# Performance work log

Hardware: AMD Instinct MI355X
Metric: run time of the kernel (lower is better)

The kernel has to match this reference:

```python
import jax, jax.numpy as jnp
import numpy as np

BUCKET_BINS = np.array([0, 1, 2, 3, 4, 5, 7, 8, 15, 16, 31, 32, 63, 64], dtype=np.int32)
MAX_WINDOW = 8  # args.span_maximum_length


def _span_index_table(L):
    # Static enumeration of all spans of width 1..MAX_WINDOW (stride-1 unfold).
    starts, ends = [], []
    for w in range(1, min(L, MAX_WINDOW) + 1):
        s = np.arange(0, L - w + 1)
        starts.append(s)
        ends.append(s + w)
    return (np.concatenate(starts).astype(np.int32),
            np.concatenate(ends).astype(np.int32))


def _bucket(width):
    # index of last bin with width >= bin value
    return jnp.searchsorted(jnp.asarray(BUCKET_BINS), width, side='right') - 1


def _fnn(h, W1, b1, W2, b2, W3, b3):
    # Linear->ReLU->(Dropout: eval identity)->Linear->ReLU->Linear->Softmax
    h = jax.nn.relu(h @ W1 + b1)
    h = jax.nn.relu(h @ W2 + b2)
    return jax.nn.softmax(h @ W3 + b3, axis=-1)


def setup_inputs() -> dict:
    key = jax.random.key(0)
    ks = jax.random.split(key, 16)
    B, L, D = 8, 256, 768
    H, WD, DD = 1024, 25, 25
    span_dim = 2 * D + WD          # 1561
    pair_dim = 2 * span_dim + DD   # 3147
    f = jnp.float32

    def g(k, shape, scale):
        return jax.random.normal(k, shape, dtype=f) * scale

    return {
        'x': g(ks[0], (B, L, D), 1.0),
        'width_emb': g(ks[1], (len(BUCKET_BINS), WD), 0.02),
        'dist_emb': g(ks[2], (len(BUCKET_BINS), DD), 0.02),
        'Ws1': g(ks[3], (span_dim, H), 0.02), 'bs1': jnp.zeros((H,), f),
        'Ws2': g(ks[4], (H, H), 0.02), 'bs2': jnp.zeros((H,), f),
        'Ws3': g(ks[5], (H, 3), 0.02), 'bs3': jnp.zeros((3,), f),
        'Wp1': g(ks[6], (pair_dim, H), 0.02), 'bp1': jnp.zeros((H,), f),
        'Wp2': g(ks[7], (H, H), 0.02), 'bp2': jnp.zeros((H,), f),
        'Wp3': g(ks[8], (H, 4), 0.02), 'bp3': jnp.zeros((4,), f),
        'nz': 64,
    }


def reference(x, width_emb, dist_emb, Ws1, bs1, Ws2, bs2, Ws3, bs3,
              Wp1, bp1, Wp2, bp2, Wp3, bp3, nz):
    B, L, D = x.shape
    starts_np, ends_np = _span_index_table(L)
    starts = jnp.asarray(starts_np)
    ends = jnp.asarray(ends_np)

    # ---- SpanRepresentation: [start token, end token, width bucket emb] ----
    w_emb = width_emb[_bucket(ends - starts)]                     # [S, WD]
    spans = jnp.concatenate([
        x[:, starts_np, :],                                       # [B,S,D]
        x[:, ends_np - 1, :],                                     # [B,S,D]
        jnp.broadcast_to(w_emb, (B,) + w_emb.shape),              # [B,S,WD]
    ], axis=-1)                                                   # [B,S,span_dim]

    # ---- span_fnn + PrunedTargetOpinion (top-k on aspect/opinion probs) ----
    span_prob = _fnn(spans, Ws1, bs1, Ws2, bs2, Ws3, bs3)         # [B,S,3]
    _, t_idx = jax.lax.top_k(span_prob[:, :, 1], nz)              # aspect  [B,nz]
    _, o_idx = jax.lax.top_k(span_prob[:, :, 2], nz)              # opinion [B,nz]

    # ---- PairRepresentation: all target x opinion pairs ----
    t_rep = jnp.take_along_axis(spans, t_idx[:, :, None], axis=1) # [B,nz,sd]
    o_rep = jnp.take_along_axis(spans, o_idx[:, :, None], axis=1)
    ta, tb = starts[t_idx], ends[t_idx]                           # [B,nz]
    oc, od = starts[o_idx], ends[o_idx]
    # min_distance(a,b,c,d) = min(|b-c|, |a-d|)
    dist = jnp.minimum(jnp.abs(tb[:, :, None] - oc[:, None, :]),
                       jnp.abs(ta[:, :, None] - od[:, None, :]))  # [B,nz,nz]
    d_emb = dist_emb[_bucket(dist)]                               # [B,nz,nz,DD]
    sd = spans.shape[-1]
    pairs = jnp.concatenate([
        jnp.broadcast_to(t_rep[:, :, None, :], (B, nz, nz, sd)),
        jnp.broadcast_to(o_rep[:, None, :, :], (B, nz, nz, sd)),
        d_emb,
    ], axis=-1).reshape(B, nz * nz, 2 * sd + d_emb.shape[-1])     # [B,nz^2,pair_dim]

    pair_prob = _fnn(pairs, Wp1, bp1, Wp2, bp2, Wp3, bp3)         # [B,nz^2,4]
    return span_prob, pair_prob
```

## Files before the change

kernel.cpp:

```cpp
#include <hip/hip_runtime.h>
#include <cstdint>
#include <cstddef>

#define BATCH 8
#define SEQ   256
#define DIM   768
#define NSPAN 2020
#define HID   1024
#define NZ    64

typedef unsigned short u16;
typedef unsigned int   u32;
typedef unsigned long long u64;

typedef __bf16 bf16x8 __attribute__((ext_vector_type(8)));
typedef float  f32x4  __attribute__((ext_vector_type(4)));

__device__ __forceinline__ u16 f2bf(float f) {
    union { float f; u32 u; } x; x.f = f;
    u32 r = x.u + 0x7fffu + ((x.u >> 16) & 1u);
    return (u16)(r >> 16);
}
__device__ __forceinline__ float bf2f(u16 b) {
    union { u32 u; float f; } x; x.u = ((u32)b) << 16;
    return x.f;
}
__device__ __forceinline__ void splitbf(float v, u16& h, u16& l) {
    h = f2bf(v);
    l = f2bf(v - bf2f(h));
}

__device__ __forceinline__ void gld_lds16(const void* g, void* l) {
    __builtin_amdgcn_global_load_lds(
        (const __attribute__((address_space(1))) unsigned int*)g,
        (__attribute__((address_space(3))) unsigned int*)l, 16, 0, 0);
}

__device__ __forceinline__ void span_decode(int s, int& start, int& end, int& w) {
    int off = 0;
#pragma unroll
    for (int wi = 1; wi <= 8; ++wi) {
        int cnt = SEQ - wi + 1;
        if (s < off + cnt) { w = wi; start = s - off; end = start + wi; return; }
        off += cnt;
    }
    w = 8; start = 0; end = 8;
}

__device__ __forceinline__ int dbucket(int d) {
    int b = 0;
    b += (d >= 1);  b += (d >= 2);  b += (d >= 3);  b += (d >= 4);
    b += (d >= 5);  b += (d >= 7);  b += (d >= 8);  b += (d >= 15);
    b += (d >= 16); b += (d >= 31); b += (d >= 32); b += (d >= 63);
    b += (d >= 64);
    return b;
}

__device__ __forceinline__ void xcd_map(int L, int sft, int& bx, int& by) {
    int grp = L >> (3 + sft);
    int rem = L & ((1 << (3 + sft)) - 1);
    bx = rem >> 3;
    by = (grp << 3) | (rem & 7);
}

__global__ __launch_bounds__(256) void k_prep(
    const float* __restrict__ x,  u16* __restrict__ xh,   u16* __restrict__ xl,
    const float* __restrict__ wemb, const float* __restrict__ demb,
    const float* __restrict__ bs1, const float* __restrict__ bp1,
    float* __restrict__ wtabS, float* __restrict__ wtabPt,
    float* __restrict__ wtabPo, float* __restrict__ dtab,
    const float* __restrict__ Ws1, u16* __restrict__ W1Th, u16* __restrict__ W1Tl,
    const float* __restrict__ Ws2, u16* __restrict__ W2Th, u16* __restrict__ W2Tl,
    const float* __restrict__ Wp2, u16* __restrict__ Wp2T,
    const float* __restrict__ Wp1, u16* __restrict__ Wp1T4)
{
    __shared__ float tile[32][33];
    const int bid = blockIdx.x, tid = threadIdx.x;
    if (bid < 6144) {
        int i = bid * 256 + tid;
        u16 h, l; splitbf(x[i], h, l);
        xh[i] = h; xl[i] = l;
        return;
    }
    if (bid < 6296) {
        int t = bid - 6144;
        int row = t >> 2;
        int h = (t & 3) * 256 + tid;
        const int wb[8] = {1,2,3,4,5,5,6,7};
        if (row < 8) {
            int bk = wb[row];
            float acc = bs1[h];
            for (int j = 0; j < 25; ++j) acc = fmaf(wemb[bk*25+j], Ws1[(size_t)(1536+j)*HID + h], acc);
            wtabS[row*HID + h] = acc;
        } else if (row < 16) {
            int bk = wb[row-8];
            float acc = 0.f;
            for (int j = 0; j < 25; ++j) acc = fmaf(wemb[bk*25+j], Wp1[(size_t)(1536+j)*HID + h], acc);
            wtabPt[(row-8)*HID + h] = acc;
        } else if (row < 24) {
            int bk = wb[row-16];
            float acc = 0.f;
            for (int j = 0; j < 25; ++j) acc = fmaf(wemb[bk*25+j], Wp1[(size_t)(3097+j)*HID + h], acc);
            wtabPo[(row-16)*HID + h] = acc;
        } else {
            int tt = row - 24;
            float acc = bp1[h];
            for (int j = 0; j < 25; ++j) acc = fmaf(demb[tt*25+j], Wp1[(size_t)(3122+j)*HID + h], acc);
            dtab[tt*HID + h] = acc;
        }
        return;
    }
    const int tb = bid - 6296;
    const int tr = tid >> 3;
    const int tc4 = (tid & 7) * 4;
    int job, tk, tn, blk = 0;
    if (tb < 1536)      { job = 0; tk = tb % 24; tn = tb / 24; }
    else if (tb < 2560) { job = 1; int t = tb - 1536; tk = t & 31; tn = t >> 5; }
    else if (tb < 3584) { job = 2; int t = tb - 2560; tk = t & 31; tn = t >> 5; }
    else                { job = 3; int t = tb - 3584; blk = t / 768; int r = t - blk * 768; tk = r % 24; tn = r / 24; }
    const int k0 = tk * 32, n0 = tn * 32;

    int k = k0 + tr;
    float4 v;
    if (job == 0) {
        const float* s = (n0 < 1024) ? (Ws1 + (size_t)k * HID + n0)
                                     : (Ws1 + (size_t)(768 + k) * HID + (n0 - 1024));
        v = *(const float4*)(s + tc4);
    } else if (job == 1) {
        v = *(const float4*)(Ws2 + (size_t)k * HID + n0 + tc4);
    } else if (job == 2) {
        v = *(const float4*)(Wp2 + (size_t)k * HID + n0 + tc4);
    } else {
        const int roff[4] = {0, 768, 1561, 2329};
        v = *(const float4*)(Wp1 + (size_t)(roff[blk] + k) * HID + n0 + tc4);
    }
    tile[tr][tc4+0] = v.x; tile[tr][tc4+1] = v.y;
    tile[tr][tc4+2] = v.z; tile[tr][tc4+3] = v.w;
    __syncthreads();

    int nn = n0 + tr;
    float w0 = tile[tc4+0][tr], w1 = tile[tc4+1][tr];
    float w2 = tile[tc4+2][tr], w3 = tile[tc4+3][tr];
    if (job == 0) {
        size_t d = (size_t)nn * 768 + k0 + tc4;
        u16 h0,l0,h1,l1,h2,l2,h3,l3;
        splitbf(w0,h0,l0); splitbf(w1,h1,l1); splitbf(w2,h2,l2); splitbf(w3,h3,l3);
        *(uint2*)(W1Th + d) = make_uint2((u32)h0 | ((u32)h1 << 16), (u32)h2 | ((u32)h3 << 16));
        *(uint2*)(W1Tl + d) = make_uint2((u32)l0 | ((u32)l1 << 16), (u32)l2 | ((u32)l3 << 16));
    } else if (job == 1) {
        size_t d = (size_t)nn * 1024 + k0 + tc4;
        u16 h0,l0,h1,l1,h2,l2,h3,l3;
        splitbf(w0,h0,l0); splitbf(w1,h1,l1); splitbf(w2,h2,l2); splitbf(w3,h3,l3);
        *(uint2*)(W2Th + d) = make_uint2((u32)h0 | ((u32)h1 << 16), (u32)h2 | ((u32)h3 << 16));
        *(uint2*)(W2Tl + d) = make_uint2((u32)l0 | ((u32)l1 << 16), (u32)l2 | ((u32)l3 << 16));
    } else if (job == 2) {
        size_t d = (size_t)nn * 1024 + k0 + tc4;
        *(uint2*)(Wp2T + d) = make_uint2((u32)f2bf(w0) | ((u32)f2bf(w1) << 16),
                                         (u32)f2bf(w2) | ((u32)f2bf(w3) << 16));
    } else {
        size_t d = (size_t)blk * 786432 + (size_t)nn * 768 + k0 + tc4;
        *(uint2*)(Wp1T4 + d) = make_uint2((u32)f2bf(w0) | ((u32)f2bf(w1) << 16),
                                          (u32)f2bf(w2) | ((u32)f2bf(w3) << 16));
    }
}

__global__ __launch_bounds__(256) void k_gemm3bf(
    const u16* __restrict__ Ah, const u16* __restrict__ Al, int lda,
    const u16* __restrict__ BTh, const u16* __restrict__ BTl, int ldb,
    float* __restrict__ C, int ldc,
    int M, int K, int nby, int sft)
{
    int bx, by;
    xcd_map(blockIdx.x, sft, bx, by);
    if (by >= nby) return;
    __shared__ __align__(16) u16 sm[4 * 128 * 32];
    u16* sAh = sm;
    u16* sAl = sm + 4096;
    u16* sBh = sm + 8192;
    u16* sBl = sm + 12288;
    const int tid = threadIdx.x;
    const int bm = by * 128, bn = bx * 128;
    const int wave = tid >> 6, lane = tid & 63;
    const int wr = wave >> 1, wc = wave & 1;
    const int q = lane >> 4, tl = lane & 15;

    f32x4 zero = {0.f, 0.f, 0.f, 0.f};
    f32x4 acc[4][4];
#pragma unroll
    for (int i = 0; i < 4; ++i)
#pragma unroll
        for (int j = 0; j < 4; ++j) acc[i][j] = zero;

    const int srow = lane >> 2;
    const int scol = (lane & 3) * 8;
    int ra0 = bm + wave * 32 + srow;      if (ra0 >= M) ra0 = M - 1;
    int ra1 = bm + wave * 32 + 16 + srow; if (ra1 >= M) ra1 = M - 1;
    const int rb0 = bn + wave * 32 + srow;
    const int rb1 = bn + wave * 32 + 16 + srow;
    u16* dA0 = sAh + wave * 1024;  u16* dA1 = dA0 + 512;
    u16* dL0 = sAl + wave * 1024;  u16* dL1 = dL0 + 512;
    u16* dB0 = sBh + wave * 1024;  u16* dB1 = dB0 + 512;
    u16* dC0 = sBl + wave * 1024;  u16* dC1 = dC0 + 512;
    const u16* gA0 = Ah  + (size_t)ra0 * lda + scol;
    const u16* gA1 = Ah  + (size_t)ra1 * lda + scol;
    const u16* gL0 = Al  + (size_t)ra0 * lda + scol;
    const u16* gL1 = Al  + (size_t)ra1 * lda + scol;
    const u16* gB0 = BTh + (size_t)rb0 * ldb + scol;
    const u16* gB1 = BTh + (size_t)rb1 * ldb + scol;
    const u16* gC0 = BTl + (size_t)rb0 * ldb + scol;
    const u16* gC1 = BTl + (size_t)rb1 * ldb + scol;

    for (int k0 = 0; k0 < K; k0 += 32) {
        gld_lds16(gA0 + k0, dA0);
        gld_lds16(gA1 + k0, dA1);
        gld_lds16(gL0 + k0, dL0);
        gld_lds16(gL1 + k0, dL1);
        gld_lds16(gB0 + k0, dB0);
        gld_lds16(gB1 + k0, dB1);
        gld_lds16(gC0 + k0, dC0);
        gld_lds16(gC1 + k0, dC1);
        __syncthreads();
        bf16x8 ah[4], al[4], bh[4], bl[4];
#pragma unroll
        for (int t = 0; t < 4; ++t) {
            int arow = (wr*64 + t*16 + tl) * 32 + q*8;
            int brow = (wc*64 + t*16 + tl) * 32 + q*8;
            ah[t] = *(const bf16x8*)(&sAh[arow]);
            al[t] = *(const bf16x8*)(&sAl[arow]);
            bh[t] = *(const bf16x8*)(&sBh[brow]);
            bl[t] = *(const bf16x8*)(&sBl[brow]);
        }
#pragma unroll
        for (int ti = 0; ti < 4; ++ti)
#pragma unroll
            for (int tj = 0; tj < 4; ++tj) {
                acc[ti][tj] = __builtin_amdgcn_mfma_f32_16x16x32_bf16(ah[ti], bh[tj], acc[ti][tj], 0, 0, 0);
                acc[ti][tj] = __builtin_amdgcn_mfma_f32_16x16x32_bf16(al[ti], bh[tj], acc[ti][tj], 0, 0, 0);
                acc[ti][tj] = __builtin_amdgcn_mfma_f32_16x16x32_bf16(ah[ti], bl[tj], acc[ti][tj], 0, 0, 0);
            }
        __syncthreads();
    }
#pragma unroll
    for (int ti = 0; ti < 4; ++ti) {
#pragma unroll
        for (int tj = 0; tj < 4; ++tj) {
            int gcol = bn + wc*64 + tj*16 + tl;
#pragma unroll
            for (int r = 0; r < 4; ++r) {
                int grow = bm + wr*64 + ti*16 + q*4 + r;
                if (grow >= M) continue;
                C[(size_t)grow * ldc + gcol] = acc[ti][tj][r];
            }
        }
    }
}

__global__ __launch_bounds__(256) void k_span_l2(
    const u16* __restrict__ Ah, const u16* __restrict__ Al,
    const u16* __restrict__ BTh, const u16* __restrict__ BTl,
    const float* __restrict__ bs2, const float* __restrict__ Ws3,
    float* __restrict__ part, int M)
{
    int bx, by;
    xcd_map(blockIdx.x, 3, bx, by);
    if (by >= 127) return;
    __shared__ __align__(16) u16 sm[4 * 128 * 32];
    u16* sAh = sm;
    u16* sAl = sm + 4096;
    u16* sBh = sm + 8192;
    u16* sBl = sm + 12288;
    const int tid = threadIdx.x;
    const int bm = by * 128, bn = bx * 128;
    const int wave = tid >> 6, lane = tid & 63;
    const int wr = wave >> 1, wc = wave & 1;
    const int q = lane >> 4, tl = lane & 15;

    f32x4 zero = {0.f, 0.f, 0.f, 0.f};
    f32x4 acc[4][4];
#pragma unroll
    for (int i = 0; i < 4; ++i)
#pragma unroll
        for (int j = 0; j < 4; ++j) acc[i][j] = zero;

    const int srow = lane >> 2;
    const int scol = (lane & 3) * 8;
    int ra0 = bm + wave * 32 + srow;      if (ra0 >= M) ra0 = M - 1;
    int ra1 = bm + wave * 32 + 16 + srow; if (ra1 >= M) ra1 = M - 1;
    const int rb0 = bn + wave * 32 + srow;
    const int rb1 = bn + wave * 32 + 16 + srow;
    u16* dA0 = sAh + wave * 1024;  u16* dA1 = dA0 + 512;
    u16* dL0 = sAl + wave * 1024;  u16* dL1 = dL0 + 512;
    u16* dB0 = sBh + wave * 1024;  u16* dB1 = dB0 + 512;
    u16* dC0 = sBl + wave * 1024;  u16* dC1 = dC0 + 512;
    const u16* gA0 = Ah  + (size_t)ra0 * HID + scol;
    const u16* gA1 = Ah  + (size_t)ra1 * HID + scol;
    const u16* gL0 = Al  + (size_t)ra0 * HID + scol;
    const u16* gL1 = Al  + (size_t)ra1 * HID + scol;
    const u16* gB0 = BTh + (size_t)rb0 * HID + scol;
    const u16* gB1 = BTh + (size_t)rb1 * HID + scol;
    const u16* gC0 = BTl + (size_t)rb0 * HID + scol;
    const u16* gC1 = BTl + (size_t)rb1 * HID + scol;

    for (int k0 = 0; k0 < HID; k0 += 32) {
        gld_lds16(gA0 + k0, dA0);
        gld_lds16(gA1 + k0, dA1);
        gld_lds16(gL0 + k0, dL0);
        gld_lds16(gL1 + k0, dL1);
        gld_lds16(gB0 + k0, dB0);
        gld_lds16(gB1 + k0, dB1);
        gld_lds16(gC0 + k0, dC0);
        gld_lds16(gC1 + k0, dC1);
        __syncthreads();
        bf16x8 ah[4], al[4], bh[4], bl[4];
#pragma unroll
        for (int t = 0; t < 4; ++t) {
            int arow = (wr*64 + t*16 + tl) * 32 + q*8;
            int brow = (wc*64 + t*16 + tl) * 32 + q*8;
            ah[t] = *(const bf16x8*)(&sAh[arow]);
            al[t] = *(const bf16x8*)(&sAl[arow]);
            bh[t] = *(const bf16x8*)(&sBh[brow]);
            bl[t] = *(const bf16x8*)(&sBl[brow]);
        }
#pragma unroll
        for (int ti = 0; ti < 4; ++ti)
#pragma unroll
            for (int tj = 0; tj < 4; ++tj) {
                acc[ti][tj] = __builtin_amdgcn_mfma_f32_16x16x32_bf16(ah[ti], bh[tj], acc[ti][tj], 0, 0, 0);
                acc[ti][tj] = __builtin_amdgcn_mfma_f32_16x16x32_bf16(al[ti], bh[tj], acc[ti][tj], 0, 0, 0);
                acc[ti][tj] = __builtin_amdgcn_mfma_f32_16x16x32_bf16(ah[ti], bl[tj], acc[ti][tj], 0, 0, 0);
            }
        __syncthreads();
    }
    const int slot = bx * 2 + wc;
#pragma unroll
    for (int ti = 0; ti < 4; ++ti) {
#pragma unroll
        for (int r = 0; r < 4; ++r) {
            int grow = bm + wr*64 + ti*16 + q*4 + r;
            float l0 = 0.f, l1 = 0.f, l2 = 0.f;
#pragma unroll
            for (int tj = 0; tj < 4; ++tj) {
                int gcol = bn + wc*64 + tj*16 + tl;
                float v = fmaxf(acc[ti][tj][r] + bs2[gcol], 0.f);
                const float* w3 = Ws3 + gcol * 3;
                l0 = fmaf(v, w3[0], l0);
                l1 = fmaf(v, w3[1], l1);
                l2 = fmaf(v, w3[2], l2);
            }
#pragma unroll
            for (int off = 8; off > 0; off >>= 1) {
                l0 += __shfl_down(l0, off, 16);
                l1 += __shfl_down(l1, off, 16);
                l2 += __shfl_down(l2, off, 16);
            }
            if (tl == 0 && grow < M) {
                float* dst = part + ((size_t)grow * 16 + slot) * 3;
                dst[0] = l0; dst[1] = l1; dst[2] = l2;
            }
        }
    }
}

__global__ __launch_bounds__(256) void k_pairL1(
    const u16* __restrict__ xh, const u16* __restrict__ Wp1T4,
    float* __restrict__ TO2, const int* __restrict__ toks)
{
    __shared__ __align__(16) u16 sm[2 * 64 * 32];
    u16* sA = sm;
    u16* sB = sm + 2048;
    const int tid = threadIdx.x;
    const int bid = blockIdx.x;
    const int p = bid >> 8;
    const int bx = bid & 15, by = (bid >> 4) & 15;
    const int bm = by * 64, bn = bx * 64;
    const int wave = tid >> 6, lane = tid & 63;
    const int wr = wave >> 1, wc = wave & 1;
    const int q = lane >> 4, tl = lane & 15;
    const bool isO = bm >= 512;

    f32x4 zero = {0.f, 0.f, 0.f, 0.f};
    f32x4 acc[2][2];
#pragma unroll
    for (int i = 0; i < 2; ++i)
#pragma unroll
        for (int j = 0; j < 2; ++j) acc[i][j] = zero;

    const int srow = tid >> 2;
    const int scol = (tid & 3) * 8;
    u16* dA = sA + wave * 512;
    u16* dB = sB + wave * 512;

    int arow = toks[bm + srow + p * 1024];
    const u16* gA = xh + (size_t)arow * DIM + scol;
    const u16* gB = Wp1T4 + ((size_t)((isO ? 2 : 0) + p) * 1024 + bn + srow) * DIM + scol;
    for (int k0 = 0; k0 < DIM; k0 += 32) {
        gld_lds16(gA + k0, dA);
        gld_lds16(gB + k0, dB);
        __syncthreads();
        bf16x8 af[2], bf[2];
#pragma unroll
        for (int t = 0; t < 2; ++t) {
            af[t] = *(const bf16x8*)(&sA[(wr*32 + t*16 + tl) * 32 + q*8]);
            bf[t] = *(const bf16x8*)(&sB[(wc*32 + t*16 + tl) * 32 + q*8]);
        }
#pragma unroll
        for (int ti = 0; ti < 2; ++ti)
#pragma unroll
            for (int tj = 0; tj < 2; ++tj)
                acc[ti][tj] = __builtin_amdgcn_mfma_f32_16x16x32_bf16(af[ti], bf[tj], acc[ti][tj], 0, 0, 0);
        __syncthreads();
    }
    float* dstb = TO2 + (size_t)p * 1024 * HID;
#pragma unroll
    for (int ti = 0; ti < 2; ++ti) {
#pragma unroll
        for (int tj = 0; tj < 2; ++tj) {
            int gcol = bn + wc*32 + tj*16 + tl;
#pragma unroll
            for (int r = 0; r < 4; ++r) {
                int grow = bm + wr*32 + ti*16 + q*4 + r;
                dstb[(size_t)grow * HID + gcol] = acc[ti][tj][r];
            }
        }
    }
}

__global__ __launch_bounds__(256) void k_build_h1s(
    const float* __restrict__ XALL, const float* __restrict__ wtabS,
    u16* __restrict__ h1h, u16* __restrict__ h1l)
{
    int r = blockIdx.x;
    int b = r / NSPAN, s = r - b * NSPAN;
    int st, en, w; span_decode(s, st, en, w);
    const float4* xs = (const float4*)(XALL + (size_t)(b*SEQ + st) * 2048);
    const float4* xe = (const float4*)(XALL + (size_t)(b*SEQ + en - 1) * 2048 + 1024);
    const float4* wt = (const float4*)(wtabS + (size_t)(w-1) * HID);
    int t = threadIdx.x;
    float4 a = xs[t], bz = xe[t], c = wt[t];
    float v0 = fmaxf(a.x + bz.x + c.x, 0.f);
    float v1 = fmaxf(a.y + bz.y + c.y, 0.f);
    float v2 = fmaxf(a.z + bz.z + c.z, 0.f);
    float v3 = fmaxf(a.w + bz.w + c.w, 0.f);
    u16 h0,l0,h1,l1,h2,l2,h3,l3;
    splitbf(v0,h0,l0); splitbf(v1,h1,l1); splitbf(v2,h2,l2); splitbf(v3,h3,l3);
    size_t base = (size_t)r * HID + t * 4;
    *(uint2*)(h1h + base) = make_uint2((u32)h0 | ((u32)h1 << 16), (u32)h2 | ((u32)h3 << 16));
    *(uint2*)(h1l + base) = make_uint2((u32)l0 | ((u32)l1 << 16), (u32)l2 | ((u32)l3 << 16));
}

__global__ __launch_bounds__(256) void k_topk(
    const float* __restrict__ partS, const float* __restrict__ bs3,
    float* __restrict__ out, int* __restrict__ t_idx, int* __restrict__ o_idx,
    int* __restrict__ toks)
{
    int b = blockIdx.x >> 1;
    int head = 1 + (blockIdx.x & 1);
    int* outp = (head == 1 ? t_idx : o_idx) + b * NZ;
    __shared__ u64 keys[2048];
    int tid = threadIdx.x;
#pragma unroll
    for (int ii = 0; ii < 8; ++ii) {
        int s = tid + ii * 256;
        u32 fb = 0;
        if (s < NSPAN) {
            const float* p = partS + (size_t)(b * NSPAN + s) * 48;
            float s0 = bs3[0], s1 = bs3[1], s2 = bs3[2];
#pragma unroll
            for (int t = 0; t < 16; ++t) {
                s0 += p[t*3]; s1 += p[t*3+1]; s2 += p[t*3+2];
            }
            float m = fmaxf(s0, fmaxf(s1, s2));
            float e0 = expf(s0 - m), e1 = expf(s1 - m), e2 = expf(s2 - m);
            float inv = 1.f / (e0 + e1 + e2);
            float p0 = e0 * inv, p1 = e1 * inv, p2 = e2 * inv;
            float* o = out + (size_t)(b * NSPAN + s) * 3;
            o[0] = p0; o[1] = p1; o[2] = p2;
            union { float f; u32 u; } x;
            x.f = (head == 1) ? p1 : p2;
            fb = x.u;
        }
        keys[s] = ((u64)fb << 32) | (u64)(0xFFFFFFFFu - (u32)s);
    }
    __syncthreads();
    for (int k = 2; k <= 2048; k <<= 1) {
        for (int j = k >> 1; j > 0; j >>= 1) {
#pragma unroll
            for (int ii = 0; ii < 8; ++ii) {
                int i = tid + ii * 256;
                int ixj = i ^ j;
                if (ixj > i) {
                    u64 a = keys[i], c = keys[ixj];
                    bool desc = (i & k) == 0;
                    bool wrong = desc ? (a < c) : (a > c);
                    if (wrong) { keys[i] = c; keys[ixj] = a; }
                }
            }
            __syncthreads();
        }
    }
    if (tid < NZ) {
        u64 key = keys[tid];
        int fi = (int)(0xFFFFFFFFu - (u32)(key & 0xFFFFFFFFu));
        if (fi < 0 || fi >= NSPAN) fi = 0;
        outp[tid] = fi;
        int st, en, w; span_decode(fi, st, en, w);
        int base = (head == 1 ? 0 : 512) + b * NZ + tid;
        toks[base] = b * SEQ + st;
        toks[1024 + base] = b * SEQ + en - 1;
    }
}

__global__ __launch_bounds__(256) void k_build_h1p(
    const float* __restrict__ TO2, const int* __restrict__ t_idx, const int* __restrict__ o_idx,
    const float* __restrict__ wtabPt, const float* __restrict__ wtabPo,
    const float* __restrict__ dtab, u16* __restrict__ h1p)
{
    __shared__ float Ts[8][HID];
    __shared__ float Os[4][HID];
    const int bid = blockIdx.x;
    const int b = bid >> 7;
    const int it = (bid >> 4) & 7;
    const int jt = bid & 15;
    const int i0 = it * 8, j0 = jt * 4;
    const int tid = threadIdx.x;
    const int k4 = tid * 4;
    const size_t PS = (size_t)1024 * HID;

    int tinfo[8][2];
    int oinfo[4][2];
#pragma unroll
    for (int r = 0; r < 8; ++r) {
        int i = i0 + r;
        int ts = t_idx[b*64 + i];
        int ta, tb, wt; span_decode(ts, ta, tb, wt);
        tinfo[r][0] = ta; tinfo[r][1] = tb;
        float4 t0 = *(const float4*)(TO2 + (size_t)(b*64 + i) * HID + k4);
        float4 t1 = *(const float4*)(TO2 + PS + (size_t)(b*64 + i) * HID + k4);
        float4 pp = *(const float4*)(wtabPt + (size_t)(wt-1) * HID + k4);
        Ts[r][k4+0] = t0.x + t1.x + pp.x;
        Ts[r][k4+1] = t0.y + t1.y + pp.y;
        Ts[r][k4+2] = t0.z + t1.z + pp.z;
        Ts[r][k4+3] = t0.w + t1.w + pp.w;
    }
#pragma unroll
    for (int r = 0; r < 4; ++r) {
        int j = j0 + r;
        int os = o_idx[b*64 + j];
        int oc, od, wo; span_decode(os, oc, od, wo);
        oinfo[r][0] = oc; oinfo[r][1] = od;
        float4 o0 = *(const float4*)(TO2 + (size_t)(512 + b*64 + j) * HID + k4);
        float4 o1 = *(const float4*)(TO2 + PS + (size_t)(512 + b*64 + j) * HID + k4);
        float4 qq = *(const float4*)(wtabPo + (size_t)(wo-1) * HID + k4);
        Os[r][k4+0] = o0.x + o1.x + qq.x;
        Os[r][k4+1] = o0.y + o1.y + qq.y;
        Os[r][k4+2] = o0.z + o1.z + qq.z;
        Os[r][k4+3] = o0.w + o1.w + qq.w;
    }
    __syncthreads();

#pragma unroll
    for (int ri = 0; ri < 8; ++ri) {
#pragma unroll
        for (int rj = 0; rj < 4; ++rj) {
            int ta = tinfo[ri][0], tb = tinfo[ri][1];
            int oc = oinfo[rj][0], od = oinfo[rj][1];
            int d1 = tb - oc; d1 = d1 < 0 ? -d1 : d1;
            int d2 = ta - od; d2 = d2 < 0 ? -d2 : d2;
            int dist = d1 < d2 ? d1 : d2;
            int db = dbucket(dist);
            const float4 dd = *(const float4*)(dtab + (size_t)db * HID + k4);
            float vx = fmaxf(Ts[ri][k4+0] + Os[rj][k4+0] + dd.x, 0.f);
            float vy = fmaxf(Ts[ri][k4+1] + Os[rj][k4+1] + dd.y, 0.f);
            float vz = fmaxf(Ts[ri][k4+2] + Os[rj][k4+2] + dd.z, 0.f);
            float vw = fmaxf(Ts[ri][k4+3] + Os[rj][k4+3] + dd.w, 0.f);
            u32 p0 = (u32)f2bf(vx) | ((u32)f2bf(vy) << 16);
            u32 p1 = (u32)f2bf(vz) | ((u32)f2bf(vw) << 16);
            int row = b * 4096 + (i0 + ri) * 64 + (j0 + rj);
            *(uint2*)(h1p + (size_t)row * HID + k4) = make_uint2(p0, p1);
        }
    }
}

__global__ __launch_bounds__(256) void k_pair_l2(
    const u16* __restrict__ Abf, const u16* __restrict__ BT,
    const float* __restrict__ bp2, const float* __restrict__ Wp3,
    float* __restrict__ part)
{
    int bx, by;
    xcd_map(blockIdx.x, 3, bx, by);
    __shared__ __align__(16) u16 sm[2 * 128 * 32];
    u16* As = sm;
    u16* Bs = sm + 4096;
    const int tid = threadIdx.x;
    const int bm = by * 128, bn = bx * 128;
    const int wave = tid >> 6, lane = tid & 63;
    const int wr = wave >> 1, wc = wave & 1;
    const int q = lane >> 4, tl = lane & 15;

    f32x4 zero = {0.f, 0.f, 0.f, 0.f};
    f32x4 acc[4][4];
#pragma unroll
    for (int i = 0; i < 4; ++i)
#pragma unroll
        for (int j = 0; j < 4; ++j) acc[i][j] = zero;

    const int srow = lane >> 2;
    const int scol = (lane & 3) * 8;
    const u16* gA0 = Abf + (size_t)(bm + wave*32 + srow) * 1024 + scol;
    const u16* gA1 = Abf + (size_t)(bm + wave*32 + 16 + srow) * 1024 + scol;
    const u16* gB0 = BT  + (size_t)(bn + wave*32 + srow) * 1024 + scol;
    const u16* gB1 = BT  + (size_t)(bn + wave*32 + 16 + srow) * 1024 + scol;
    u16* dA0 = As + wave * 1024;  u16* dA1 = dA0 + 512;
    u16* dB0 = Bs + wave * 1024;  u16* dB1 = dB0 + 512;

    for (int k0 = 0; k0 < 1024; k0 += 32) {
        gld_lds16(gA0 + k0, dA0);
        gld_lds16(gA1 + k0, dA1);
        gld_lds16(gB0 + k0, dB0);
        gld_lds16(gB1 + k0, dB1);
        __syncthreads();
        bf16x8 af[4], bf[4];
#pragma unroll
        for (int t = 0; t < 4; ++t) {
            af[t] = *(const bf16x8*)(&As[(wr*64 + t*16 + tl) * 32 + q*8]);
            bf[t] = *(const bf16x8*)(&Bs[(wc*64 + t*16 + tl) * 32 + q*8]);
        }
#pragma unroll
        for (int ti = 0; ti < 4; ++ti)
#pragma unroll
            for (int tj = 0; tj < 4; ++tj)
                acc[ti][tj] = __builtin_amdgcn_mfma_f32_16x16x32_bf16(af[ti], bf[tj], acc[ti][tj], 0, 0, 0);
        __syncthreads();
    }
    const int slot = bx * 2 + wc;
#pragma unroll
    for (int ti = 0; ti < 4; ++ti) {
#pragma unroll
        for (int r = 0; r < 4; ++r) {
            int grow = bm + wr*64 + ti*16 + q*4 + r;
            float l0 = 0.f, l1 = 0.f, l2 = 0.f, l3 = 0.f;
#pragma unroll
            for (int tj = 0; tj < 4; ++tj) {
                int gcol = bn + wc*64 + tj*16 + tl;
                float v = fmaxf(acc[ti][tj][r] + bp2[gcol], 0.f);
                const float4 w = *(const float4*)(Wp3 + gcol * 4);
                l0 = fmaf(v, w.x, l0); l1 = fmaf(v, w.y, l1);
                l2 = fmaf(v, w.z, l2); l3 = fmaf(v, w.w, l3);
            }
#pragma unroll
            for (int off = 8; off > 0; off >>= 1) {
                l0 += __shfl_down(l0, off, 16);
                l1 += __shfl_down(l1, off, 16);
                l2 += __shfl_down(l2, off, 16);
                l3 += __shfl_down(l3, off, 16);
            }
            if (tl == 0) {
                float* dst = part + ((size_t)grow * 16 + slot) * 4;
                dst[0] = l0; dst[1] = l1; dst[2] = l2; dst[3] = l3;
            }
        }
    }
}

__global__ __launch_bounds__(256) void k_pair_red(
    const float* __restrict__ part, const float* __restrict__ bp3,
    float* __restrict__ out)
{
    int r = blockIdx.x * 256 + threadIdx.x;
    const float4* p = (const float4*)(part + (size_t)r * 64);
    float s0 = bp3[0], s1 = bp3[1], s2 = bp3[2], s3 = bp3[3];
#pragma unroll
    for (int t = 0; t < 16; ++t) {
        float4 v = p[t];
        s0 += v.x; s1 += v.y; s2 += v.z; s3 += v.w;
    }
    float m = fmaxf(fmaxf(s0, s1), fmaxf(s2, s3));
    float e0 = expf(s0 - m), e1 = expf(s1 - m), e2 = expf(s2 - m), e3 = expf(s3 - m);
    float inv = 1.f / (e0 + e1 + e2 + e3);
    float* o = out + (size_t)r * 4;
    o[0] = e0 * inv; o[1] = e1 * inv; o[2] = e2 * inv; o[3] = e3 * inv;
}

extern "C" void kernel_launch(void* const* d_in, const int* in_sizes, int n_in,
                              void* d_out, int out_size, void* d_ws, size_t ws_size,
                              hipStream_t stream)
{
    const float* x    = (const float*)d_in[0];
    const float* wemb = (const float*)d_in[1];
    const float* demb = (const float*)d_in[2];
    const float* Ws1  = (const float*)d_in[3];
    const float* bs1  = (const float*)d_in[4];
    const float* Ws2  = (const float*)d_in[5];
    const float* bs2  = (const float*)d_in[6];
    const float* Ws3  = (const float*)d_in[7];
    const float* bs3  = (const float*)d_in[8];
    const float* Wp1  = (const float*)d_in[9];
    const float* bp1  = (const float*)d_in[10];
    const float* Wp2  = (const float*)d_in[11];
    const float* bp2  = (const float*)d_in[12];
    const float* Wp3  = (const float*)d_in[13];
    const float* bp3  = (const float*)d_in[14];
    float* out = (float*)d_out;
    char* ws = (char*)d_ws;

    const size_t RSZ = (size_t)32768 * HID * 2;
    size_t off = 0;
    auto alloc = [&](size_t bytes) -> void* {
        void* p = ws + off;
        off += (bytes + 255) & ~(size_t)255;
        return p;
    };
    char* R1 = (char*)alloc(RSZ);
    char* R2 = (char*)alloc(RSZ);
    u16*   h1h  = (u16*)R1;
    u16*   h1l  = (u16*)(R1 + (size_t)16160 * HID * 2);
    float* XALL = (float*)R2;
    u16*   xl   = (u16*)(R2 + (16u << 20));
    u16*   W1Th = (u16*)(R2 + (19u << 20));
    u16*   W1Tl = (u16*)(R2 + (22u << 20));
    u16*   h1p  = (u16*)R2;
    u16*   xh     = (u16*)alloc((size_t)2048 * DIM * 2);
    float* TO2    = (float*)alloc((size_t)2 * 1024 * HID * 4);
    float* partS  = (float*)alloc((size_t)16160 * 16 * 3 * 4);
    float* partP  = (float*)alloc((size_t)32768 * 16 * 4 * 4);
    u16*   W2Th   = (u16*)alloc((size_t)1024 * 1024 * 2);
    u16*   W2Tl   = (u16*)alloc((size_t)1024 * 1024 * 2);
    u16*   Wp2T   = (u16*)alloc((size_t)1024 * 1024 * 2);
    u16*   Wp1T4  = (u16*)alloc((size_t)4 * 1024 * 768 * 2);
    float* wtabS  = (float*)alloc(8 * HID * 4);
    float* wtabPt = (float*)alloc(8 * HID * 4);
    float* wtabPo = (float*)alloc(8 * HID * 4);
    float* dtab   = (float*)alloc(14 * HID * 4);
    int*   t_idx  = (int*)alloc(BATCH * NZ * 4);
    int*   o_idx  = (int*)alloc(BATCH * NZ * 4);
    int*   toks   = (int*)alloc(2048 * 4);
    (void)ws_size; (void)in_sizes; (void)n_in; (void)out_size;

    k_prep<<<12952, 256, 0, stream>>>(x, xh, xl, wemb, demb, bs1, bp1,
                                      wtabS, wtabPt, wtabPo, dtab,
                                      Ws1, W1Th, W1Tl, Ws2, W2Th, W2Tl,
                                      Wp2, Wp2T, Wp1, Wp1T4);

    k_gemm3bf<<<256, 256, 0, stream>>>(xh, xl, 768, W1Th, W1Tl, 768,
                                       XALL, 2048, 2048, 768, 16, 4);
    k_build_h1s<<<16160, 256, 0, stream>>>(XALL, wtabS, h1h, h1l);
    k_span_l2<<<1024, 256, 0, stream>>>(h1h, h1l, W2Th, W2Tl, bs2, Ws3, partS, 16160);
    k_topk<<<16, 256, 0, stream>>>(partS, bs3, out, t_idx, o_idx, toks);
    k_pairL1<<<512, 256, 0, stream>>>(xh, Wp1T4, TO2, toks);
    k_build_h1p<<<1024, 256, 0, stream>>>(TO2, t_idx, o_idx, wtabPt, wtabPo, dtab, h1p);
    k_pair_l2<<<2048, 256, 0, stream>>>(h1p, Wp2T, bp2, Wp3, partP);
    k_pair_red<<<128, 256, 0, stream>>>(partP, bp3, out + 48480);
}
```

Before: 467.1 us.

## Retile span and pair layer-2 GEMMs to 256x256 with double-buffered swizzled LDS

Both layer-2 GEMM kernels move from 128x128 tiles with 256 threads to 256x256 tiles with 512 threads (8 waves, each computing 128x64). They double-buffer LDS so the global-to-LDS prefetch of the next K step overlaps the MFMA work, and they use raw vmcnt waits and barriers instead of two __syncthreads per step. The LDS layout gets an XOR swizzle to reduce bank conflicts, s_setprio is raised around the MFMA block, and the block-index mapping is swizzled for XCD locality. Costs are 128 KB of LDS per block and higher register pressure from 32 accumulators per wave. With the new 2048-row-aligned span tiling, the bound check depends on clamping rows to M-1.

Result: slower. 485.5 us (+3.9%).

```diff
diff --git a/kernel.cpp b/kernel.cpp
--- a/kernel.cpp
+++ b/kernel.cpp
@@ -255,93 +255,99 @@
     }
 }
 
-__global__ __launch_bounds__(256) void k_span_l2(
+__global__ __launch_bounds__(512, 2) void k_span_l2(
     const u16* __restrict__ Ah, const u16* __restrict__ Al,
     const u16* __restrict__ BTh, const u16* __restrict__ BTl,
     const float* __restrict__ bs2, const float* __restrict__ Ws3,
     float* __restrict__ part, int M)
 {
-    int bx, by;
-    xcd_map(blockIdx.x, 3, bx, by);
-    if (by >= 127) return;
-    __shared__ __align__(16) u16 sm[4 * 128 * 32];
-    u16* sAh = sm;
-    u16* sAl = sm + 4096;
-    u16* sBh = sm + 8192;
-    u16* sBl = sm + 12288;
+    __shared__ __align__(16) u16 sm[65536];
     const int tid = threadIdx.x;
-    const int bm = by * 128, bn = bx * 128;
+    const int swz = (blockIdx.x & 7) * 32 + (blockIdx.x >> 3);
+    const int by = swz >> 2, bx = swz & 3;
+    const int bm = by * 256, bn = bx * 256;
     const int wave = tid >> 6, lane = tid & 63;
-    const int wr = wave >> 1, wc = wave & 1;
-    const int q = lane >> 4, tl = lane & 15;
+    const int wm = wave >> 2, wn = wave & 3;
+    const int tl = lane & 15, q8 = lane >> 4;
+
+    const int sr  = lane >> 2;
+    const int scs = lane & 3;
+    const int scl = scs ^ ((sr >> 1) & 3);
+    const u16* gsrc[8];
+    u32 ldst[8];
+#pragma unroll
+    for (int j = 0; j < 8; ++j) {
+        int G = j * 8 + wave;
+        int arr  = G >> 4;
+        int half = (G >> 3) & 1;
+        int sb   = G & 7;
+        int row = ((arr < 2) ? bm : bn) + half * 128 + sb * 16 + sr;
+        if (arr < 2 && row >= M) row = M - 1;
+        const u16* base = (arr == 0) ? Ah : (arr == 1) ? Al : (arr == 2) ? BTh : BTl;
+        gsrc[j] = base + (size_t)row * HID + scl * 8;
+        ldst[j] = arr * 8192 + half * 4096 + sb * 512;
+    }
+    const int cpr = q8 ^ ((tl >> 1) & 3);
+    const u32 lof = (u32)(tl * 32 + cpr * 8);
+    const u32 rA  = (u32)(wm * 4096) + lof;
+    const u32 rB  = 16384u + (u32)((wn >> 1) * 4096 + (wn & 1) * 2048) + lof;
 
     f32x4 zero = {0.f, 0.f, 0.f, 0.f};
-    f32x4 acc[4][4];
-#pragma unroll
-    for (int i = 0; i < 4; ++i)
+    f32x4 acc[8][4];
+#pragma unroll
+    for (int i = 0; i < 8; ++i)
 #pragma unroll
         for (int j = 0; j < 4; ++j) acc[i][j] = zero;
 
-    const int srow = lane >> 2;
-    const int scol = (lane & 3) * 8;
-    int ra0 = bm + wave * 32 + srow;      if (ra0 >= M) ra0 = M - 1;
-    int ra1 = bm + wave * 32 + 16 + srow; if (ra1 >= M) ra1 = M - 1;
-    const int rb0 = bn + wave * 32 + srow;
-    const int rb1 = bn + wave * 32 + 16 + srow;
-    u16* dA0 = sAh + wave * 1024;  u16* dA1 = dA0 + 512;
-    u16* dL0 = sAl + wave * 1024;  u16* dL1 = dL0 + 512;
-    u16* dB0 = sBh + wave * 1024;  u16* dB1 = dB0 + 512;
-    u16* dC0 = sBl + wave * 1024;  u16* dC1 = dC0 + 512;
-    const u16* gA0 = Ah  + (size_t)ra0 * HID + scol;
-    const u16* gA1 = Ah  + (size_t)ra1 * HID + scol;
-    const u16* gL0 = Al  + (size_t)ra0 * HID + scol;
-    const u16* gL1 = Al  + (size_t)ra1 * HID + scol;
-    const u16* gB0 = BTh + (size_t)rb0 * HID + scol;
-    const u16* gB1 = BTh + (size_t)rb1 * HID + scol;
-    const u16* gC0 = BTl + (size_t)rb0 * HID + scol;
-    const u16* gC1 = BTl + (size_t)rb1 * HID + scol;
-
-    for (int k0 = 0; k0 < HID; k0 += 32) {
-        gld_lds16(gA0 + k0, dA0);
-        gld_lds16(gA1 + k0, dA1);
-        gld_lds16(gL0 + k0, dL0);
-        gld_lds16(gL1 + k0, dL1);
-        gld_lds16(gB0 + k0, dB0);
-        gld_lds16(gB1 + k0, dB1);
-        gld_lds16(gC0 + k0, dC0);
-        gld_lds16(gC1 + k0, dC1);
-        __syncthreads();
-        bf16x8 ah[4], al[4], bh[4], bl[4];
-#pragma unroll
-        for (int t = 0; t < 4; ++t) {
-            int arow = (wr*64 + t*16 + tl) * 32 + q*8;
-            int brow = (wc*64 + t*16 + tl) * 32 + q*8;
-            ah[t] = *(const bf16x8*)(&sAh[arow]);
-            al[t] = *(const bf16x8*)(&sAl[arow]);
-            bh[t] = *(const bf16x8*)(&sBh[brow]);
-            bl[t] = *(const bf16x8*)(&sBl[brow]);
-        }
-#pragma unroll
-        for (int ti = 0; ti < 4; ++ti)
-#pragma unroll
-            for (int tj = 0; tj < 4; ++tj) {
-                acc[ti][tj] = __builtin_amdgcn_mfma_f32_16x16x32_bf16(ah[ti], bh[tj], acc[ti][tj], 0, 0, 0);
-                acc[ti][tj] = __builtin_amdgcn_mfma_f32_16x16x32_bf16(al[ti], bh[tj], acc[ti][tj], 0, 0, 0);
-                acc[ti][tj] = __builtin_amdgcn_mfma_f32_16x16x32_bf16(ah[ti], bl[tj], acc[ti][tj], 0, 0, 0);
-            }
-        __syncthreads();
-    }
-    const int slot = bx * 2 + wc;
-#pragma unroll
-    for (int ti = 0; ti < 4; ++ti) {
+#pragma unroll
+    for (int j = 0; j < 8; ++j) gld_lds16(gsrc[j], sm + ldst[j]);
+
+    for (int t = 0; t < 32; ++t) {
+        const u32 bufo = (u32)(t & 1) * 32768u;
+        if (t < 31) {
+            const int k0 = (t + 1) * 32;
+            const u32 nb = bufo ^ 32768u;
+#pragma unroll
+            for (int j = 0; j < 8; ++j) gld_lds16(gsrc[j] + k0, sm + nb + ldst[j]);
+            asm volatile("s_waitcnt vmcnt(8)" ::: "memory");
+        } else {
+            asm volatile("s_waitcnt vmcnt(0)" ::: "memory");
+        }
+        asm volatile("s_barrier" ::: "memory");
+
+        bf16x8 bh[4], bl[4];
+#pragma unroll
+        for (int fn = 0; fn < 4; ++fn) {
+            bh[fn] = *(const bf16x8*)(sm + bufo + rB + fn * 512);
+            bl[fn] = *(const bf16x8*)(sm + bufo + rB + 8192 + fn * 512);
+        }
+        __builtin_amdgcn_s_setprio(1);
+#pragma unroll
+        for (int fm = 0; fm < 8; ++fm) {
+            bf16x8 ah = *(const bf16x8*)(sm + bufo + rA + fm * 512);
+            bf16x8 al = *(const bf16x8*)(sm + bufo + rA + 8192 + fm * 512);
+#pragma unroll
+            for (int fn = 0; fn < 4; ++fn) {
+                acc[fm][fn] = __builtin_amdgcn_mfma_f32_16x16x32_bf16(ah, bh[fn], acc[fm][fn], 0, 0, 0);
+                acc[fm][fn] = __builtin_amdgcn_mfma_f32_16x16x32_bf16(al, bh[fn], acc[fm][fn], 0, 0, 0);
+                acc[fm][fn] = __builtin_amdgcn_mfma_f32_16x16x32_bf16(ah, bl[fn], acc[fm][fn], 0, 0, 0);
+            }
+        }
+        __builtin_amdgcn_s_setprio(0);
+        asm volatile("s_barrier" ::: "memory");
+    }
+
+    const int slot = bx * 4 + wn;
+#pragma unroll
+    for (int fm = 0; fm < 8; ++fm) {
 #pragma unroll
         for (int r = 0; r < 4; ++r) {
-            int grow = bm + wr*64 + ti*16 + q*4 + r;
+            int grow = bm + wm * 128 + fm * 16 + q8 * 4 + r;
             float l0 = 0.f, l1 = 0.f, l2 = 0.f;
 #pragma unroll
-            for (int tj = 0; tj < 4; ++tj) {
-                int gcol = bn + wc*64 + tj*16 + tl;
-                float v = fmaxf(acc[ti][tj][r] + bs2[gcol], 0.f);
+            for (int fn = 0; fn < 4; ++fn) {
+                int gcol = bn + wn * 64 + fn * 16 + tl;
+                float v = fmaxf(acc[fm][fn][r] + bs2[gcol], 0.f);
                 const float* w3 = Ws3 + gcol * 3;
                 l0 = fmaf(v, w3[0], l0);
                 l1 = fmaf(v, w3[1], l1);
@@ -581,68 +587,97 @@
     }
 }
 
-__global__ __launch_bounds__(256) void k_pair_l2(
+__global__ __launch_bounds__(512, 2) void k_pair_l2(
     const u16* __restrict__ Abf, const u16* __restrict__ BT,
     const float* __restrict__ bp2, const float* __restrict__ Wp3,
     float* __restrict__ part)
 {
-    int bx, by;
-    xcd_map(blockIdx.x, 3, bx, by);
-    __shared__ __align__(16) u16 sm[2 * 128 * 32];
-    u16* As = sm;
-    u16* Bs = sm + 4096;
+    __shared__ __align__(16) u16 sm[65536];
     const int tid = threadIdx.x;
-    const int bm = by * 128, bn = bx * 128;
+    const int swz = (blockIdx.x & 7) * 64 + (blockIdx.x >> 3);
+    const int by = swz >> 2, bx = swz & 3;
+    const int bm = by * 256, bn = bx * 256;
     const int wave = tid >> 6, lane = tid & 63;
-    const int wr = wave >> 1, wc = wave & 1;
-    const int q = lane >> 4, tl = lane & 15;
+    const int wm = wave >> 2, wn = wave & 3;
+    const int tl = lane & 15, q8 = lane >> 4;
+
+    const int sr  = lane >> 2;
+    const int scs = lane & 3;
+    const int scl = scs ^ ((sr >> 1) & 3);
+    const u16* gsrc[8];
+    u32 ldst[8];
+#pragma unroll
+    for (int j = 0; j < 8; ++j) {
+        int G = j * 8 + wave;
+        int arr  = G >> 5;
+        int half = (G >> 4) & 1;
+        int sb   = G & 15;
+        int row = (arr ? bn : bm) + half * 128 + (sb >> 1) * 16 + sr;
+        int ks  = sb & 1;
+        const u16* base = arr ? BT : Abf;
+        gsrc[j] = base + (size_t)row * HID + ks * 32 + scl * 8;
+        ldst[j] = arr * 16384 + half * 8192 + sb * 512;
+    }
+    const int cpr = q8 ^ ((tl >> 1) & 3);
+    const u32 lof = (u32)(tl * 32 + cpr * 8);
+    const u32 rA  = (u32)(wm * 8192) + lof;
+    const u32 rB  = 16384u + (u32)((wn >> 1) * 8192 + (wn & 1) * 4096) + lof;
 
     f32x4 zero = {0.f, 0.f, 0.f, 0.f};
-    f32x4 acc[4][4];
-#pragma unroll
-    for (int i = 0; i < 4; ++i)
+    f32x4 acc[8][4];
+#pragma unroll
+    for (int i = 0; i < 8; ++i)
 #pragma unroll
         for (int j = 0; j < 4; ++j) acc[i][j] = zero;
 
-    const int srow = lane >> 2;
-    const int scol = (lane & 3) * 8;
-    const u16* gA0 = Abf + (size_t)(bm + wave*32 + srow) * 1024 + scol;
-    const u16* gA1 = Abf + (size_t)(bm + wave*32 + 16 + srow) * 1024 + scol;
-    const u16* gB0 = BT  + (size_t)(bn + wave*32 + srow) * 1024 + scol;
-    const u16* gB1 = BT  + (size_t)(bn + wave*32 + 16 + srow) * 1024 + scol;
-    u16* dA0 = As + wave * 1024;  u16* dA1 = dA0 + 512;
-    u16* dB0 = Bs + wave * 1024;  u16* dB1 = dB0 + 512;
-
-    for (int k0 = 0; k0 < 1024; k0 += 32) {
-        gld_lds16(gA0 + k0, dA0);
-        gld_lds16(gA1 + k0, dA1);
-        gld_lds16(gB0 + k0, dB0);
-        gld_lds16(gB1 + k0, dB1);
-        __syncthreads();
-        bf16x8 af[4], bf[4];
-#pragma unroll
-        for (int t = 0; t < 4; ++t) {
-            af[t] = *(const bf16x8*)(&As[(wr*64 + t*16 + tl) * 32 + q*8]);
-            bf[t] = *(const bf16x8*)(&Bs[(wc*64 + t*16 + tl) * 32 + q*8]);
-        }
-#pragma unroll
-        for (int ti = 0; ti < 4; ++ti)
-#pragma unroll
-            for (int tj = 0; tj < 4; ++tj)
-                acc[ti][tj] = __builtin_amdgcn_mfma_f32_16x16x32_bf16(af[ti], bf[tj], acc[ti][tj], 0, 0, 0);
-        __syncthreads();
-    }
-    const int slot = bx * 2 + wc;
-#pragma unroll
-    for (int ti = 0; ti < 4; ++ti) {
+#pragma unroll
+    for (int j = 0; j < 8; ++j) gld_lds16(gsrc[j], sm + ldst[j]);
+
+    for (int t = 0; t < 16; ++t) {
+        const u32 bufo = (u32)(t & 1) * 32768u;
+        if (t < 15) {
+            const int k0 = (t + 1) * 64;
+            const u32 nb = bufo ^ 32768u;
+#pragma unroll
+            for (int j = 0; j < 8; ++j) gld_lds16(gsrc[j] + k0, sm + nb + ldst[j]);
+            asm volatile("s_waitcnt vmcnt(8)" ::: "memory");
+        } else {
+            asm volatile("s_waitcnt vmcnt(0)" ::: "memory");
+        }
+        asm volatile("s_barrier" ::: "memory");
+
+        bf16x8 b0[4], b1[4];
+#pragma unroll
+        for (int fn = 0; fn < 4; ++fn) {
+            b0[fn] = *(const bf16x8*)(sm + bufo + rB + (fn * 2 + 0) * 512);
+            b1[fn] = *(const bf16x8*)(sm + bufo + rB + (fn * 2 + 1) * 512);
+        }
+        __builtin_amdgcn_s_setprio(1);
+#pragma unroll
+        for (int fm = 0; fm < 8; ++fm) {
+            bf16x8 a0 = *(const bf16x8*)(sm + bufo + rA + (fm * 2 + 0) * 512);
+            bf16x8 a1 = *(const bf16x8*)(sm + bufo + rA + (fm * 2 + 1) * 512);
+#pragma unroll
+            for (int fn = 0; fn < 4; ++fn) {
+                acc[fm][fn] = __builtin_amdgcn_mfma_f32_16x16x32_bf16(a0, b0[fn], acc[fm][fn], 0, 0, 0);
+                acc[fm][fn] = __builtin_amdgcn_mfma_f32_16x16x32_bf16(a1, b1[fn], acc[fm][fn], 0, 0, 0);
+            }
+        }
+        __builtin_amdgcn_s_setprio(0);
+        asm volatile("s_barrier" ::: "memory");
+    }
+
+    const int slot = bx * 4 + wn;
+#pragma unroll
+    for (int fm = 0; fm < 8; ++fm) {
 #pragma unroll
         for (int r = 0; r < 4; ++r) {
-            int grow = bm + wr*64 + ti*16 + q*4 + r;
+            int grow = bm + wm * 128 + fm * 16 + q8 * 4 + r;
             float l0 = 0.f, l1 = 0.f, l2 = 0.f, l3 = 0.f;
 #pragma unroll
-            for (int tj = 0; tj < 4; ++tj) {
-                int gcol = bn + wc*64 + tj*16 + tl;
-                float v = fmaxf(acc[ti][tj][r] + bp2[gcol], 0.f);
+            for (int fn = 0; fn < 4; ++fn) {
+                int gcol = bn + wn * 64 + fn * 16 + tl;
+                float v = fmaxf(acc[fm][fn][r] + bp2[gcol], 0.f);
                 const float4 w = *(const float4*)(Wp3 + gcol * 4);
                 l0 = fmaf(v, w.x, l0); l1 = fmaf(v, w.y, l1);
                 l2 = fmaf(v, w.z, l2); l3 = fmaf(v, w.w, l3);
@@ -744,10 +779,10 @@
     k_gemm3bf<<<256, 256, 0, stream>>>(xh, xl, 768, W1Th, W1Tl, 768,
                                        XALL, 2048, 2048, 768, 16, 4);
     k_build_h1s<<<16160, 256, 0, stream>>>(XALL, wtabS, h1h, h1l);
-    k_span_l2<<<1024, 256, 0, stream>>>(h1h, h1l, W2Th, W2Tl, bs2, Ws3, partS, 16160);
+    k_span_l2<<<256, 512, 0, stream>>>(h1h, h1l, W2Th, W2Tl, bs2, Ws3, partS, 16160);
     k_topk<<<16, 256, 0, stream>>>(partS, bs3, out, t_idx, o_idx, toks);
     k_pairL1<<<512, 256, 0, stream>>>(xh, Wp1T4, TO2, toks);
     k_build_h1p<<<1024, 256, 0, stream>>>(TO2, t_idx, o_idx, wtabPt, wtabPo, dtab, h1p);
-    k_pair_l2<<<2048, 256, 0, stream>>>(h1p, Wp2T, bp2, Wp3, partP);
+    k_pair_l2<<<512, 512, 0, stream>>>(h1p, Wp2T, bp2, Wp3, partP);
     k_pair_red<<<128, 256, 0, stream>>>(partP, bp3, out + 48480);
 }
```
